# Optimization experiments

Measured on AMD Instinct MI355X. Metric: run time of the kernel, lower is better.

The kernel has to match this reference:

```python
import jax, jax.numpy as jnp
import numpy as np

N = 50000        # nodes
E = 800000       # edges (before self-loops)
IN = 128         # in_dim
H = 2            # heads
C1 = 64          # hidden_dim (per head)
D1 = H * C1      # conv1 concat output = 128
OUT = 64         # out_dim
C2 = 2 * OUT     # conv2 per-head channels = 128 (concat=False -> mean over heads)
NEG = 0.2        # GATv2 leaky_relu negative slope
EPS = 1e-5       # BatchNorm eps


def setup_inputs() -> dict:
    key = jax.random.key(0)
    ks = jax.random.split(key, 14)
    s = 0.05
    inp = {
        "x": jax.random.normal(ks[0], (N, IN), jnp.float32),
        "edge_index": jax.random.randint(ks[1], (2, E), 0, N, dtype=jnp.int32),
        # conv1 (GATv2: lin_l for source, lin_r for target, att vector per head)
        "W_l1": jax.random.normal(ks[2], (IN, D1), jnp.float32) * s,
        "b_l1": jnp.zeros((D1,), jnp.float32),
        "W_r1": jax.random.normal(ks[3], (IN, D1), jnp.float32) * s,
        "b_r1": jnp.zeros((D1,), jnp.float32),
        "att1": jax.random.normal(ks[4], (H, C1), jnp.float32) * s,
        "bias1": jnp.zeros((D1,), jnp.float32),
        # batch_norm1 (affine)
        "gamma1": jnp.ones((D1,), jnp.float32),
        "beta1": jnp.zeros((D1,), jnp.float32),
        # conv2
        "W_l2": jax.random.normal(ks[5], (D1, H * C2), jnp.float32) * s,
        "b_l2": jnp.zeros((H * C2,), jnp.float32),
        "W_r2": jax.random.normal(ks[6], (D1, H * C2), jnp.float32) * s,
        "b_r2": jnp.zeros((H * C2,), jnp.float32),
        "att2": jax.random.normal(ks[7], (H, C2), jnp.float32) * s,
        "bias2": jnp.zeros((C2,), jnp.float32),
    }
    return inp


def gatv2_layer(x, src, dst, W_l, b_l, W_r, b_r, att, bias, concat):
    Hh, Cc = att.shape
    x_l = (x @ W_l + b_l).reshape(N, Hh, Cc)   # source transform
    x_r = (x @ W_r + b_r).reshape(N, Hh, Cc)   # target transform
    # per-edge GATv2 score: att . leaky_relu(x_l[j] + x_r[i])
    e = jax.nn.leaky_relu(x_l[src] + x_r[dst], NEG)      # [E', H, C]
    logit = jnp.einsum("ehc,hc->eh", e, att)              # [E', H]
    # segment softmax over incoming edges of each target node
    m = jax.ops.segment_max(logit, dst, num_segments=N)   # [N, H]
    ex = jnp.exp(logit - m[dst])
    den = jax.ops.segment_sum(ex, dst, num_segments=N)    # [N, H]
    alpha = ex / den[dst]                                  # [E', H]
    out = jax.ops.segment_sum(x_l[src] * alpha[:, :, None], dst, num_segments=N)
    out = out.reshape(N, Hh * Cc) if concat else out.mean(axis=1)
    return out + bias


def batchnorm(x, gamma=None, beta=None):
    mu = x.mean(axis=0)
    var = x.var(axis=0)  # biased variance, as used by BN for normalization
    xn = (x - mu) * jax.lax.rsqrt(var + EPS)
    if gamma is not None:
        xn = xn * gamma + beta
    return xn


def reference(x, edge_index, W_l1, b_l1, W_r1, b_r1, att1, bias1, gamma1, beta1,
              W_l2, b_l2, W_r2, b_r2, att2, bias2):
    loops = jnp.arange(N, dtype=edge_index.dtype)
    src = jnp.concatenate([edge_index[0], loops])  # add self-loops (PyG default)
    dst = jnp.concatenate([edge_index[1], loops])
    h = gatv2_layer(x, src, dst, W_l1, b_l1, W_r1, b_r1, att1, bias1, True)
    h = jax.nn.relu(batchnorm(h, gamma1, beta1))
    o = gatv2_layer(h, src, dst, W_l2, b_l2, W_r2, b_r2, att2, bias2, False)
    mu_part = batchnorm(o[:, :OUT])                      # affine=False
    return jnp.concatenate([mu_part, jax.nn.softplus(o[:, OUT:])], axis=1)
```

## Files before the change

kernel.cpp:

```cpp
#include <hip/hip_runtime.h>
#include <hip/hip_bf16.h>
#include <math.h>

#define NNODES 50000
#define NEDGES 800000
#define EPTOT  (NEDGES + NNODES)
#define NEG_SLOPE 0.2f
#define BN_EPS 1e-5f
#define LOG2E 1.44269504088896f
#define ESLOT 64

#define PB_SC  3321
#define PB_W1  (PB_SC + 128)
#define PB_W2  (PB_W1 + 256)

typedef __hip_bfloat16 bf16;
typedef __attribute__((ext_vector_type(8))) short short8;
typedef __attribute__((ext_vector_type(4))) float f32x4;
typedef __attribute__((ext_vector_type(2))) float f32x2;

__device__ __forceinline__ unsigned short f2us(float f){
    return (unsigned short)(__bfloat16_as_ushort(__float2bfloat16(f)));
}
__device__ __forceinline__ f32x2 unpk(unsigned int w){
    union { unsigned int u; float f; } lo, hi;
    lo.u = w << 16; hi.u = w & 0xffff0000u;
    f32x2 r; r.x = lo.f; r.y = hi.f; return r;
}
__device__ __forceinline__ f32x2 pkmax(f32x2 a, f32x2 b){
#if __has_builtin(__builtin_elementwise_max)
    return __builtin_elementwise_max(a, b);
#else
    f32x2 r; r.x = fmaxf(a.x, b.x); r.y = fmaxf(a.y, b.y); return r;
#endif
}
__device__ __forceinline__ unsigned int pack2(float a, float b){
    return (unsigned int)f2us(a) | ((unsigned int)f2us(b) << 16);
}

template<int CTRL>
__device__ __forceinline__ float dppadd(float v){
    int p = __builtin_amdgcn_update_dpp(0, __float_as_int(v), CTRL, 0xf, 0xf, true);
    return v + __int_as_float(p);
}
template<int G>
__device__ __forceinline__ float group_sum(float v){
    if constexpr (G == 16){
        v = dppadd<0x121>(v);
        v = dppadd<0x122>(v);
        v = dppadd<0x124>(v);
        v = dppadd<0x128>(v);
    } else {
        v = dppadd<0xB1>(v);
        v = dppadd<0x4E>(v);
        v += __shfl_xor(v, 4, 64);
    }
    return v;
}


__global__ __launch_bounds__(256) void misc_prep(
    const int* __restrict__ ei, int* __restrict__ cnt, int* __restrict__ esrc,
    const float* __restrict__ Wl1, const float* __restrict__ Wr1,
    const float* __restrict__ bl1, const float* __restrict__ br1,
    bf16* __restrict__ WT1, float* __restrict__ bc1,
    const float* __restrict__ Wl2, const float* __restrict__ Wr2,
    const float* __restrict__ bl2, const float* __restrict__ br2,
    bf16* __restrict__ WT2, float* __restrict__ bc2)
{
    int b = blockIdx.x;
    if (b < PB_SC){
        int e = b * 256 + threadIdx.x;
        if (e < EPTOT){
            int s, d;
            if (e < NEDGES){ s = ei[e]; d = ei[NEDGES + e]; } else { s = d = e - NEDGES; }
            int pos = atomicAdd(&cnt[d], 1);
            if (pos < ESLOT) esrc[(d << 6) + pos] = s;
        }
    } else if (b < PB_W1){
        int i = (b - PB_SC) * 256 + threadIdx.x;
        int r = i >> 7, k = i & 127;
        const float* W = (r < 128) ? Wl1 : Wr1;
        int c = (r < 128) ? r : r - 128;
        WT1[i] = __float2bfloat16(W[k * 128 + c]);
        if (k == 0) bc1[r] = (r < 128) ? bl1[c] : br1[c];
    } else {
        int i = (b - PB_W1) * 256 + threadIdx.x;
        int r = i >> 7, k = i & 127;
        const float* W = (r < 256) ? Wl2 : Wr2;
        int c = (r < 256) ? r : r - 256;
        WT2[i] = __float2bfloat16(W[k * 256 + c]);
        if (k == 0) bc2[r] = (r < 256) ? bl2[c] : br2[c];
    }
}


template<int DTOT, int AMODE, int NT>
__global__ __launch_bounds__(128) void mfma_gemm(
    const void* __restrict__ A, const bf16* __restrict__ WT,
    const float* __restrict__ biascat,
    bf16* __restrict__ xl, bf16* __restrict__ xr,
    const float* __restrict__ bns, const float* __restrict__ gamma,
    const float* __restrict__ beta)
{
    int wave = threadIdx.x >> 6;
    int lane = threadIdx.x & 63;
    int quad = lane >> 4;
    int l16  = lane & 15;
    int m0 = blockIdx.x * 128 + wave * 64;
    const float* Af = (const float*)A;
    const unsigned int* Ao = (const unsigned int*)A;
    const short* Bp = (const short*)WT;

    short8 af[4][4];
    #pragma unroll
    for (int k = 0; k < 4; ++k){
        float sc[8], sh[8];
        if (AMODE == 2){
            const float inv_n = 1.f / (float)NNODES;
            int cb = k * 32 + quad * 8;
            #pragma unroll
            for (int j = 0; j < 8; ++j){
                float mu = bns[cb + j] * inv_n;
                float s  = gamma[cb + j] * rsqrtf(bns[128 + cb + j] * inv_n - mu * mu + BN_EPS);
                sc[j] = s; sh[j] = beta[cb + j] - mu * s;
            }
        }
        #pragma unroll
        for (int mt = 0; mt < 4; ++mt){
            int m = m0 + mt * 16 + l16;
            m = (m < NNODES) ? m : (NNODES - 1);
            if (AMODE == 1){
                float4 v0 = *(const float4*)(Af + (size_t)m * 128 + k * 32 + quad * 8);
                float4 v1 = *(const float4*)(Af + (size_t)m * 128 + k * 32 + quad * 8 + 4);
                unsigned int* u = (unsigned int*)&af[k][mt];
                u[0] = pack2(v0.x, v0.y); u[1] = pack2(v0.z, v0.w);
                u[2] = pack2(v1.x, v1.y); u[3] = pack2(v1.z, v1.w);
            } else {
                uint4 w = *(const uint4*)(Ao + (size_t)m * 64 + k * 16 + quad * 4);
                f32x2 v0 = unpk(w.x), v1 = unpk(w.y), v2 = unpk(w.z), v3 = unpk(w.w);
                float f0 = v0.x * sc[0] + sh[0], f1 = v0.y * sc[1] + sh[1];
                float f2 = v1.x * sc[2] + sh[2], f3 = v1.y * sc[3] + sh[3];
                float f4 = v2.x * sc[4] + sh[4], f5 = v2.y * sc[5] + sh[5];
                float f6 = v3.x * sc[6] + sh[6], f7 = v3.y * sc[7] + sh[7];
                f0 = f0 > 0.f ? f0 : 0.f; f1 = f1 > 0.f ? f1 : 0.f;
                f2 = f2 > 0.f ? f2 : 0.f; f3 = f3 > 0.f ? f3 : 0.f;
                f4 = f4 > 0.f ? f4 : 0.f; f5 = f5 > 0.f ? f5 : 0.f;
                f6 = f6 > 0.f ? f6 : 0.f; f7 = f7 > 0.f ? f7 : 0.f;
                unsigned int* u = (unsigned int*)&af[k][mt];
                u[0] = pack2(f0, f1); u[1] = pack2(f2, f3);
                u[2] = pack2(f4, f5); u[3] = pack2(f6, f7);
            }
        }
    }

    for (int t = 0; t < NT; ++t){
        int n0 = (blockIdx.y * NT + t) * 64;
        f32x4 acc[4][4] = {};
        #pragma unroll
        for (int k = 0; k < 4; ++k){
            short8 bfr[4];
            #pragma unroll
            for (int nt = 0; nt < 4; ++nt){
                int n = n0 + nt * 16 + l16;
                bfr[nt] = *(const short8*)(Bp + (size_t)n * 128 + k * 32 + quad * 8);
            }
            #pragma unroll
            for (int mt = 0; mt < 4; ++mt)
                #pragma unroll
                for (int nt = 0; nt < 4; ++nt)
                    acc[mt][nt] = __builtin_amdgcn_mfma_f32_16x16x32_bf16(af[k][mt], bfr[nt], acc[mt][nt], 0, 0, 0);
        }
        #pragma unroll
        for (int nt = 0; nt < 4; ++nt){
            int n = n0 + nt * 16 + l16;
            float bi = biascat[n];
            bf16* outp = (n < DTOT) ? xl : xr;
            int c = (n < DTOT) ? n : n - DTOT;
            #pragma unroll
            for (int mt = 0; mt < 4; ++mt)
                #pragma unroll
                for (int r = 0; r < 4; ++r){
                    int m = m0 + mt * 16 + quad * 4 + r;
                    if (m < NNODES)
                        outp[(size_t)m * DTOT + c] = __float2bfloat16(acc[mt][nt][r] + bi);
                }
        }
    }
}


template<int C, bool MEAN>
__global__ __launch_bounds__(256) void gat_aggregate(
    const bf16* __restrict__ xl, const bf16* __restrict__ xr,
    const float* __restrict__ att, const int* __restrict__ cnt,
    const int* __restrict__ esrc, void* __restrict__ outv,
    const float* __restrict__ bias2)
{
    constexpr int GH  = C / 8;
    constexpr int LPE = 2 * GH;
    constexpr int EL  = 64 / LPE;
    constexpr int RB  = 4 * C;
    int lane = threadIdx.x & 63;
    int wave = threadIdx.x >> 6;
    int n    = blockIdx.x * 4 + wave;
    int el   = lane / LPE;
    int h    = (lane / GH) & 1;
    int cl   = lane % GH;
    int rowoff = h * (C * 2) + cl * 16;
    const char* xlp = (const char*)xl;

    int srcAll = esrc[(n << 6) + lane];
    int cc = cnt[n];
    int c = (cc < ESLOT) ? cc : ESLOT;
    uint4 xw = *(const uint4*)((const char*)xr + (unsigned)n * RB + rowoff);
    f32x2 xr0 = unpk(xw.x), xr1 = unpk(xw.y), xr2v = unpk(xw.z), xr3 = unpk(xw.w);
    const float* ap = att + h * C + cl * 8;
    f32x2 av0 = {ap[0] * LOG2E, ap[1] * LOG2E};
    f32x2 av1 = {ap[2] * LOG2E, ap[3] * LOG2E};
    f32x2 av2 = {ap[4] * LOG2E, ap[5] * LOG2E};
    f32x2 av3 = {ap[6] * LOG2E, ap[7] * LOG2E};
    float b2r[8];
    if (MEAN){
        #pragma unroll
        for (int v = 0; v < 8; ++v) b2r[v] = bias2[cl * 8 + v];
    }

    float den = 0.f;
    f32x2 a0 = {0.f,0.f}, a1 = {0.f,0.f}, a2 = {0.f,0.f}, a3 = {0.f,0.f};

    int ia0 = el, ib0 = EL + el;
    int sa = __shfl(srcAll, (ia0 < c) ? ia0 : (c - 1), 64);
    int sb = __shfl(srcAll, (ib0 < c) ? ib0 : (c - 1), 64);

    int p = 0;
    for (; p + EL < c; p += 2 * EL){
        uint4 wa = *(const uint4*)(xlp + ((unsigned)sa * (unsigned)RB + rowoff));
        uint4 wb = *(const uint4*)(xlp + ((unsigned)sb * (unsigned)RB + rowoff));
        float mkb = (p + EL + el < c) ? 0.f : -1e30f;

        int pn = p + 2 * EL;
        int ian = pn + el, ibn = pn + EL + el;
        int sa_n = __shfl(srcAll, (ian < c) ? ian : (c - 1), 64);
        int sb_n = __shfl(srcAll, (ibn < c) ? ibn : (c - 1), 64);

        f32x2 xa0 = unpk(wa.x), xa1 = unpk(wa.y), xa2 = unpk(wa.z), xa3 = unpk(wa.w);
        f32x2 xb0 = unpk(wb.x), xb1 = unpk(wb.y), xb2 = unpk(wb.z), xb3 = unpk(wb.w);

        f32x2 ua0 = xa0 + xr0, ua1 = xa1 + xr1, ua2 = xa2 + xr2v, ua3 = xa3 + xr3;
        f32x2 ub0 = xb0 + xr0, ub1 = xb1 + xr1, ub2 = xb2 + xr2v, ub3 = xb3 + xr3;

        f32x2 ppa = pkmax(ua0, ua0 * NEG_SLOPE) * av0;
        ppa += pkmax(ua1, ua1 * NEG_SLOPE) * av1;
        ppa += pkmax(ua2, ua2 * NEG_SLOPE) * av2;
        ppa += pkmax(ua3, ua3 * NEG_SLOPE) * av3;
        f32x2 ppb = pkmax(ub0, ub0 * NEG_SLOPE) * av0;
        ppb += pkmax(ub1, ub1 * NEG_SLOPE) * av1;
        ppb += pkmax(ub2, ub2 * NEG_SLOPE) * av2;
        ppb += pkmax(ub3, ub3 * NEG_SLOPE) * av3;
        float parta = group_sum<GH>(ppa.x + ppa.y);
        float partb = group_sum<GH>(ppb.x + ppb.y);
        float exa = exp2f(parta);
        float exb = exp2f(partb + mkb);
        den += exa + exb;
        f32x2 ea = {exa, exa}, eb = {exb, exb};
        a0 += ea * xa0; a1 += ea * xa1; a2 += ea * xa2; a3 += ea * xa3;
        a0 += eb * xb0; a1 += eb * xb1; a2 += eb * xb2; a3 += eb * xb3;
        sa = sa_n; sb = sb_n;
    }
    if (p < c){
        float mka = (p + el < c) ? 0.f : -1e30f;
        uint4 wa = *(const uint4*)(xlp + ((unsigned)sa * (unsigned)RB + rowoff));

        f32x2 xa0 = unpk(wa.x), xa1 = unpk(wa.y), xa2 = unpk(wa.z), xa3 = unpk(wa.w);
        f32x2 ua0 = xa0 + xr0, ua1 = xa1 + xr1, ua2 = xa2 + xr2v, ua3 = xa3 + xr3;

        f32x2 ppa = pkmax(ua0, ua0 * NEG_SLOPE) * av0;
        ppa += pkmax(ua1, ua1 * NEG_SLOPE) * av1;
        ppa += pkmax(ua2, ua2 * NEG_SLOPE) * av2;
        ppa += pkmax(ua3, ua3 * NEG_SLOPE) * av3;
        float parta = group_sum<GH>(ppa.x + ppa.y);
        float exa = exp2f(parta + mka);
        den += exa;
        f32x2 ea = {exa, exa};
        a0 += ea * xa0; a1 += ea * xa1; a2 += ea * xa2; a3 += ea * xa3;
    }

    #pragma unroll
    for (int mask = LPE; mask < 64; mask <<= 1){
        den  += __shfl_xor(den, mask, 64);
        a0.x += __shfl_xor(a0.x, mask, 64); a0.y += __shfl_xor(a0.y, mask, 64);
        a1.x += __shfl_xor(a1.x, mask, 64); a1.y += __shfl_xor(a1.y, mask, 64);
        a2.x += __shfl_xor(a2.x, mask, 64); a2.y += __shfl_xor(a2.y, mask, 64);
        a3.x += __shfl_xor(a3.x, mask, 64); a3.y += __shfl_xor(a3.y, mask, 64);
    }
    float inv = 1.f / den;

    if (!MEAN){
        if (el == 0){
            uint4 o;
            o.x = pack2(a0.x * inv, a0.y * inv);
            o.y = pack2(a1.x * inv, a1.y * inv);
            o.z = pack2(a2.x * inv, a2.y * inv);
            o.w = pack2(a3.x * inv, a3.y * inv);
            *(uint4*)((char*)outv + (size_t)n * RB + rowoff) = o;
        }
    } else {
        float v0 = a0.x * inv, v1 = a0.y * inv, v2 = a1.x * inv, v3 = a1.y * inv;
        float v4 = a2.x * inv, v5 = a2.y * inv, v6 = a3.x * inv, v7 = a3.y * inv;
        v0 = 0.5f * (v0 + __shfl_xor(v0, 16, 64)) + b2r[0];
        v1 = 0.5f * (v1 + __shfl_xor(v1, 16, 64)) + b2r[1];
        v2 = 0.5f * (v2 + __shfl_xor(v2, 16, 64)) + b2r[2];
        v3 = 0.5f * (v3 + __shfl_xor(v3, 16, 64)) + b2r[3];
        v4 = 0.5f * (v4 + __shfl_xor(v4, 16, 64)) + b2r[4];
        v5 = 0.5f * (v5 + __shfl_xor(v5, 16, 64)) + b2r[5];
        v6 = 0.5f * (v6 + __shfl_xor(v6, 16, 64)) + b2r[6];
        v7 = 0.5f * (v7 + __shfl_xor(v7, 16, 64)) + b2r[7];
        if (el == 0 && h == 0){
            float* outp = (float*)outv + (size_t)n * C + cl * 8;
            float4 w0 = {v0, v1, v2, v3};
            float4 w1 = {v4, v5, v6, v7};
            *(float4*)(outp) = w0;
            *(float4*)(outp + 4) = w1;
        }
    }
}


__global__ void bn_stats_bf16(const unsigned int* __restrict__ x, float* __restrict__ sums){
    __shared__ float ls[1024];
    int t = threadIdx.x;
    int c2 = t & 63;
    int rg = t >> 6;
    float s0 = 0.f, q0 = 0.f, s1 = 0.f, q1 = 0.f;
    for (int r = blockIdx.x * 4 + rg; r < NNODES; r += gridDim.x * 4){
        f32x2 v = unpk(x[(size_t)r * 64 + c2]);
        s0 += v.x; q0 += v.x * v.x;
        s1 += v.y; q1 += v.y * v.y;
    }
    ls[t] = s0; ls[256 + t] = q0; ls[512 + t] = s1; ls[768 + t] = q1;
    __syncthreads();
    if (rg == 0){
        for (int g = 1; g < 4; ++g){
            s0 += ls[g * 64 + c2];       q0 += ls[256 + g * 64 + c2];
            s1 += ls[512 + g * 64 + c2]; q1 += ls[768 + g * 64 + c2];
        }
        atomicAdd(&sums[2 * c2], s0);
        atomicAdd(&sums[128 + 2 * c2], q0);
        atomicAdd(&sums[2 * c2 + 1], s1);
        atomicAdd(&sums[128 + 2 * c2 + 1], q1);
    }
}

__global__ void bn_stats_o2(const float* __restrict__ x, float* __restrict__ sums){
    __shared__ float ls[512];
    int t = threadIdx.x;
    int col = t & 63;
    int rg  = t >> 6;
    float s = 0.f, q = 0.f;
    for (int r = blockIdx.x * 4 + rg; r < NNODES; r += gridDim.x * 4){
        float v = x[(size_t)r * 128 + col];
        s += v; q += v * v;
    }
    ls[t] = s; ls[256 + t] = q;
    __syncthreads();
    if (rg == 0){
        for (int g = 1; g < 4; ++g){ s += ls[g * 64 + col]; q += ls[256 + g * 64 + col]; }
        atomicAdd(&sums[col], s);
        atomicAdd(&sums[64 + col], q);
    }
}

__global__ void final_out(const float* __restrict__ o2, const float* __restrict__ sums,
                          float* __restrict__ out){
    int i = blockIdx.x * blockDim.x + threadIdx.x;
    if (i >= NNODES * 32) return;
    float4 v = *(const float4*)(o2 + (size_t)i * 4);
    int c = (i * 4) & 127;
    const float* vp = (const float*)&v;
    float4 r;
    float* rp = (float*)&r;
    if (c < 64){
        const float inv_n = 1.f / (float)NNODES;
        #pragma unroll
        for (int k = 0; k < 4; ++k){
            float mu = sums[c + k] * inv_n;
            float rsig = rsqrtf(sums[64 + c + k] * inv_n - mu * mu + BN_EPS);
            rp[k] = (vp[k] - mu) * rsig;
        }
    } else {
        #pragma unroll
        for (int k = 0; k < 4; ++k){
            float x = vp[k];
            rp[k] = (x > 20.f) ? x : log1pf(__expf(x));
        }
    }
    *(float4*)(out + (size_t)i * 4) = r;
}


extern "C" void kernel_launch(void* const* d_in, const int* in_sizes, int n_in,
                              void* d_out, int out_size, void* d_ws, size_t ws_size,
                              hipStream_t stream) {
    const float* x     = (const float*)d_in[0];
    const int*   ei    = (const int*)d_in[1];
    const float* W_l1  = (const float*)d_in[2];
    const float* b_l1  = (const float*)d_in[3];
    const float* W_r1  = (const float*)d_in[4];
    const float* b_r1  = (const float*)d_in[5];
    const float* att1  = (const float*)d_in[6];
    const float* gamma1 = (const float*)d_in[8];
    const float* beta1  = (const float*)d_in[9];
    const float* W_l2  = (const float*)d_in[10];
    const float* b_l2  = (const float*)d_in[11];
    const float* W_r2  = (const float*)d_in[12];
    const float* b_r2  = (const float*)d_in[13];
    const float* att2  = (const float*)d_in[14];
    const float* bias2 = (const float*)d_in[15];
    float* out = (float*)d_out;

    char* w = (char*)d_ws;
    size_t off = 0;
    auto alloc = [&](size_t bytes) -> void* {
        void* p = w + off;
        off += (bytes + 255) & ~(size_t)255;
        return p;
    };
    const size_t NF  = (size_t)NNODES * 128 * 4;
    bf16*  xl1   = (bf16*) alloc(NF / 2);
    bf16*  xr1   = (bf16*) alloc(NF / 2);
    bf16*  xl2   = (bf16*) alloc(NF);
    bf16*  xr2   = (bf16*) alloc(NF);
    unsigned int* o1 = (unsigned int*)alloc(NF / 2);
    float* o2    = (float*)alloc(NF);
    bf16*  WT1   = (bf16*) alloc(256 * 128 * 2);
    bf16*  WT2   = (bf16*) alloc(512 * 128 * 2);
    float* bc1   = (float*)alloc(256 * 4);
    float* bc2   = (float*)alloc(512 * 4);
    int*   cnt    = (int*)  alloc((size_t)NNODES * 4);
    int*   esrc   = (int*)  alloc((size_t)NNODES * ESLOT * 4);
    float* bnsums = (float*)alloc(384 * 4);
    float* bn1s = bnsums;
    float* bn2s = bnsums + 256;

    hipMemsetAsync(cnt, 0, (size_t)NNODES * 4, stream);
    hipMemsetAsync(bnsums, 0, 384 * 4, stream);

    misc_prep<<<PB_W2, 256, 0, stream>>>(ei, cnt, esrc,
                                         W_l1, W_r1, b_l1, b_r1, WT1, bc1,
                                         W_l2, W_r2, b_l2, b_r2, WT2, bc2);

    mfma_gemm<128, 1, 2><<<dim3(392, 2), 128, 0, stream>>>(x, WT1, bc1, xl1, xr1,
                                                           nullptr, nullptr, nullptr);
    gat_aggregate<64, false><<<NNODES / 4, 256, 0, stream>>>(xl1, xr1, att1, cnt, esrc, o1, bias2);

    bn_stats_bf16<<<512, 256, 0, stream>>>(o1, bn1s);

    mfma_gemm<256, 2, 2><<<dim3(392, 4), 128, 0, stream>>>(o1, WT2, bc2, xl2, xr2,
                                                           bn1s, gamma1, beta1);
    gat_aggregate<128, true><<<NNODES / 4, 256, 0, stream>>>(xl2, xr2, att2, cnt, esrc, o2, bias2);

    bn_stats_o2<<<512, 256, 0, stream>>>(o2, bn2s);
    final_out<<<(NNODES * 32 + 255) / 256, 256, 0, stream>>>(o2, bn2s, out);
}
```

Baseline: 401.6 us.

## Fuse edge scatter into first GEMM launch and prefetch gathered rows in aggregation

Edge bucketing (the atomic scatter into per-node slots) moves out of the prep kernel and into extra blocks of the first MFMA GEMM launch, so scatter and GEMM1 blocks can run concurrently instead of the GEMM waiting for the full scatter. In the aggregation loop, the gathered source-row loads for the next edge pair are issued before the current pair is computed, giving software-pipelined prefetch. The costs are higher register pressure from the prefetch buffers and a larger, mixed-workload grid for GEMM1. Scatter blocks are indexed after the GEMM blocks, so they may get scheduled late.

```diff
diff --git a/kernel.cpp b/kernel.cpp
--- a/kernel.cpp
+++ b/kernel.cpp
@@ -10,9 +10,10 @@
 #define LOG2E 1.44269504088896f
 #define ESLOT 64
 
-#define PB_SC  3321
-#define PB_W1  (PB_SC + 128)
+#define PB_W1  128
 #define PB_W2  (PB_W1 + 256)
+#define GEMM1_GX 392
+#define SCAT_BX  3321
 
 typedef __hip_bfloat16 bf16;
 typedef __attribute__((ext_vector_type(8))) short short8;
@@ -60,7 +61,6 @@
 
 
 __global__ __launch_bounds__(256) void misc_prep(
-    const int* __restrict__ ei, int* __restrict__ cnt, int* __restrict__ esrc,
     const float* __restrict__ Wl1, const float* __restrict__ Wr1,
     const float* __restrict__ bl1, const float* __restrict__ br1,
     bf16* __restrict__ WT1, float* __restrict__ bc1,
@@ -69,16 +69,8 @@
     bf16* __restrict__ WT2, float* __restrict__ bc2)
 {
     int b = blockIdx.x;
-    if (b < PB_SC){
-        int e = b * 256 + threadIdx.x;
-        if (e < EPTOT){
-            int s, d;
-            if (e < NEDGES){ s = ei[e]; d = ei[NEDGES + e]; } else { s = d = e - NEDGES; }
-            int pos = atomicAdd(&cnt[d], 1);
-            if (pos < ESLOT) esrc[(d << 6) + pos] = s;
-        }
-    } else if (b < PB_W1){
-        int i = (b - PB_SC) * 256 + threadIdx.x;
+    if (b < PB_W1){
+        int i = b * 256 + threadIdx.x;
         int r = i >> 7, k = i & 127;
         const float* W = (r < 128) ? Wl1 : Wr1;
         int c = (r < 128) ? r : r - 128;
@@ -95,14 +87,26 @@
 }
 
 
-template<int DTOT, int AMODE, int NT>
+template<int DTOT, int AMODE, int NT, bool SCATTER>
 __global__ __launch_bounds__(128) void mfma_gemm(
     const void* __restrict__ A, const bf16* __restrict__ WT,
     const float* __restrict__ biascat,
     bf16* __restrict__ xl, bf16* __restrict__ xr,
     const float* __restrict__ bns, const float* __restrict__ gamma,
-    const float* __restrict__ beta)
+    const float* __restrict__ beta,
+    const int* __restrict__ ei, int* __restrict__ cnt, int* __restrict__ esrc)
 {
+    if (SCATTER && blockIdx.x >= GEMM1_GX){
+        int e = ((blockIdx.x - GEMM1_GX) * 2 + blockIdx.y) * 128 + threadIdx.x;
+        if (e < EPTOT){
+            int s, d;
+            if (e < NEDGES){ s = ei[e]; d = ei[NEDGES + e]; } else { s = d = e - NEDGES; }
+            int pos = atomicAdd(&cnt[d], 1);
+            if (pos < ESLOT) esrc[(d << 6) + pos] = s;
+        }
+        return;
+    }
+
     int wave = threadIdx.x >> 6;
     int lane = threadIdx.x & 63;
     int quad = lane >> 4;
@@ -229,20 +233,25 @@
     float den = 0.f;
     f32x2 a0 = {0.f,0.f}, a1 = {0.f,0.f}, a2 = {0.f,0.f}, a3 = {0.f,0.f};
 
-    int ia0 = el, ib0 = EL + el;
-    int sa = __shfl(srcAll, (ia0 < c) ? ia0 : (c - 1), 64);
-    int sb = __shfl(srcAll, (ib0 < c) ? ib0 : (c - 1), 64);
+    int i0 = el, i1 = EL + el;
+    int sa = __shfl(srcAll, (i0 < c) ? i0 : (c - 1), 64);
+    int sb = __shfl(srcAll, (i1 < c) ? i1 : (c - 1), 64);
+    uint4 wa = *(const uint4*)(xlp + ((unsigned)sa * (unsigned)RB + rowoff));
+    uint4 wb = *(const uint4*)(xlp + ((unsigned)sb * (unsigned)RB + rowoff));
 
     int p = 0;
     for (; p + EL < c; p += 2 * EL){
-        uint4 wa = *(const uint4*)(xlp + ((unsigned)sa * (unsigned)RB + rowoff));
-        uint4 wb = *(const uint4*)(xlp + ((unsigned)sb * (unsigned)RB + rowoff));
         float mkb = (p + EL + el < c) ? 0.f : -1e30f;
-
         int pn = p + 2 * EL;
-        int ian = pn + el, ibn = pn + EL + el;
-        int sa_n = __shfl(srcAll, (ian < c) ? ian : (c - 1), 64);
-        int sb_n = __shfl(srcAll, (ibn < c) ? ibn : (c - 1), 64);
+        uint4 wa_n, wb_n;
+        bool pf = pn < c;
+        if (pf){
+            int ian = pn + el, ibn = pn + EL + el;
+            int sa_n = __shfl(srcAll, (ian < c) ? ian : (c - 1), 64);
+            int sb_n = __shfl(srcAll, (ibn < c) ? ibn : (c - 1), 64);
+            wa_n = *(const uint4*)(xlp + ((unsigned)sa_n * (unsigned)RB + rowoff));
+            wb_n = *(const uint4*)(xlp + ((unsigned)sb_n * (unsigned)RB + rowoff));
+        }
 
         f32x2 xa0 = unpk(wa.x), xa1 = unpk(wa.y), xa2 = unpk(wa.z), xa3 = unpk(wa.w);
         f32x2 xb0 = unpk(wb.x), xb1 = unpk(wb.y), xb2 = unpk(wb.z), xb3 = unpk(wb.w);
@@ -266,12 +275,10 @@
         f32x2 ea = {exa, exa}, eb = {exb, exb};
         a0 += ea * xa0; a1 += ea * xa1; a2 += ea * xa2; a3 += ea * xa3;
         a0 += eb * xb0; a1 += eb * xb1; a2 += eb * xb2; a3 += eb * xb3;
-        sa = sa_n; sb = sb_n;
+        if (pf){ wa = wa_n; wb = wb_n; }
     }
     if (p < c){
         float mka = (p + el < c) ? 0.f : -1e30f;
-        uint4 wa = *(const uint4*)(xlp + ((unsigned)sa * (unsigned)RB + rowoff));
-
         f32x2 xa0 = unpk(wa.x), xa1 = unpk(wa.y), xa2 = unpk(wa.z), xa3 = unpk(wa.w);
         f32x2 ua0 = xa0 + xr0, ua1 = xa1 + xr1, ua2 = xa2 + xr2v, ua3 = xa3 + xr3;
 
@@ -446,18 +453,17 @@
     hipMemsetAsync(cnt, 0, (size_t)NNODES * 4, stream);
     hipMemsetAsync(bnsums, 0, 384 * 4, stream);
 
-    misc_prep<<<PB_W2, 256, 0, stream>>>(ei, cnt, esrc,
-                                         W_l1, W_r1, b_l1, b_r1, WT1, bc1,
+    misc_prep<<<PB_W2, 256, 0, stream>>>(W_l1, W_r1, b_l1, b_r1, WT1, bc1,
                                          W_l2, W_r2, b_l2, b_r2, WT2, bc2);
 
-    mfma_gemm<128, 1, 2><<<dim3(392, 2), 128, 0, stream>>>(x, WT1, bc1, xl1, xr1,
-                                                           nullptr, nullptr, nullptr);
+    mfma_gemm<128, 1, 2, true><<<dim3(GEMM1_GX + SCAT_BX, 2), 128, 0, stream>>>(
+        x, WT1, bc1, xl1, xr1, nullptr, nullptr, nullptr, ei, cnt, esrc);
     gat_aggregate<64, false><<<NNODES / 4, 256, 0, stream>>>(xl1, xr1, att1, cnt, esrc, o1, bias2);
 
     bn_stats_bf16<<<512, 256, 0, stream>>>(o1, bn1s);
 
-    mfma_gemm<256, 2, 2><<<dim3(392, 4), 128, 0, stream>>>(o1, WT2, bc2, xl2, xr2,
-                                                           bn1s, gamma1, beta1);
+    mfma_gemm<256, 2, 2, false><<<dim3(392, 4), 128, 0, stream>>>(
+        o1, WT2, bc2, xl2, xr2, bn1s, gamma1, beta1, nullptr, nullptr, nullptr);
     gat_aggregate<128, true><<<NNODES / 4, 256, 0, stream>>>(xl2, xr2, att2, cnt, esrc, o2, bias2);
 
     bn_stats_o2<<<512, 256, 0, stream>>>(o2, bn2s);
```

Measured after the change: 386.6 us. 3.8% less time.
